# Performance work log

Hardware: AMD Instinct MI355X
Metric: run time of the kernel (lower is better)

## Reference

```python
import jax, jax.numpy as jnp
import numpy as np

EMBED_DIM = 1024
VALUE_DIM = 2048
NUM_HEADS = 8
KEY_DIM = EMBED_DIM // NUM_HEADS      # 128
HEAD_DIM = VALUE_DIM // NUM_HEADS     # 256
B, T = 2, 2048
EPS = 1e-6


def _rotate_every_two(x):
    # x: [..., d] with d even; pairs (x0,x1)->(-x1,x0)
    x1 = x[..., ::2]
    x2 = x[..., 1::2]
    return jnp.stack((-x2, x1), axis=-1).reshape(x.shape)


def _theta_shift(x, sin, cos):
    # sin/cos: [T, key_dim] broadcast over [B, H, T, key_dim]
    return x * cos + _rotate_every_two(x) * sin


def setup_inputs() -> dict:
    key = jax.random.key(0)
    ks = jax.random.split(key, 6)
    x = jax.random.normal(ks[0], (B, T, EMBED_DIM), dtype=jnp.float32)

    # rotary angles as in torchscale RetNetRelPos
    angle = 1.0 / (10000.0 ** jnp.linspace(0.0, 1.0, KEY_DIM // 2))
    angle = jnp.repeat(angle, 2)                       # [key_dim], interleaved pairs
    idx = jnp.arange(T, dtype=jnp.float32)
    sin = jnp.sin(idx[:, None] * angle[None, :])       # [T, key_dim]
    cos = jnp.cos(idx[:, None] * angle[None, :])

    # per-head decay mask, normalized by sqrt(row-sum) as in RetNet
    decay = jnp.log(1.0 - 2.0 ** (-5.0 - jnp.arange(NUM_HEADS, dtype=jnp.float32)))
    diff = idx[:, None] - idx[None, :]                 # [T, T]
    exponent = jnp.where(diff >= 0, decay[:, None, None] * diff[None], -jnp.inf)
    mask = jnp.exp(exponent)                           # [H, T, T], lower-triangular decay
    mask = mask / jnp.sqrt(mask.sum(-1, keepdims=True))

    s = 0.02
    Wq = s * jax.random.normal(ks[1], (EMBED_DIM, EMBED_DIM), dtype=jnp.float32)
    Wk = s * jax.random.normal(ks[2], (EMBED_DIM, EMBED_DIM), dtype=jnp.float32)
    Wv = s * jax.random.normal(ks[3], (EMBED_DIM, VALUE_DIM), dtype=jnp.float32)
    Wg = s * jax.random.normal(ks[4], (EMBED_DIM, VALUE_DIM), dtype=jnp.float32)
    Wo = s * jax.random.normal(ks[5], (VALUE_DIM, EMBED_DIM), dtype=jnp.float32)
    return {"x": x, "sin": sin, "cos": cos, "mask": mask,
            "Wq": Wq, "Wk": Wk, "Wv": Wv, "Wg": Wg, "Wo": Wo}


def reference(x, sin, cos, mask, Wq, Wk, Wv, Wg, Wo):
    bsz, tgt_len, _ = x.shape
    scaling = KEY_DIM ** (-0.5)

    q = x @ Wq
    k = (x @ Wk) * scaling
    v = x @ Wv
    g = x @ Wg

    q = q.reshape(bsz, tgt_len, NUM_HEADS, KEY_DIM).transpose(0, 2, 1, 3)  # [B,H,T,kd]
    k = k.reshape(bsz, tgt_len, NUM_HEADS, KEY_DIM).transpose(0, 2, 1, 3)
    qr = _theta_shift(q, sin, cos)
    kr = _theta_shift(k, sin, cos)

    vr = v.reshape(bsz, tgt_len, NUM_HEADS, HEAD_DIM).transpose(0, 2, 1, 3)  # [B,H,T,hd]

    # parallel retention: decay-masked QK^T with abs-sum normalization (detached)
    qk = jnp.einsum('bhtd,bhsd->bhts', qr, kr) * mask[None]
    denom = jnp.clip(jnp.sum(jnp.abs(jax.lax.stop_gradient(qk)), axis=-1, keepdims=True),
                     1.0, 50000.0)
    qk = qk / denom
    out = jnp.einsum('bhts,bhsd->bhtd', qk, vr)          # [B,H,T,hd]
    out = out.transpose(0, 2, 1, 3)                      # [B,T,H,hd]

    # per-head RMSNorm (no affine)
    out = out * jax.lax.rsqrt(jnp.mean(out * out, axis=-1, keepdims=True) + EPS)
    out = out.reshape(bsz, tgt_len, VALUE_DIM)

    out = jax.nn.silu(g) * out
    return out @ Wo
```

## Files before the change

### kernel.cpp

```cpp
#include <hip/hip_runtime.h>
#include <hip/hip_bf16.h>
#include <math.h>

constexpr int T_SEQ = 2048;
constexpr int BB    = 2;
constexpr int EMBED = 1024;
constexpr int VDIM  = 2048;
constexpr int NHEADS = 8;
constexpr int KDIM  = 128;
constexpr int HDIM  = 256;
constexpr int ROWS  = BB * T_SEQ;
constexpr int NALL  = 6144;
constexpr float EPS = 1e-6f;

typedef float  f32x4  __attribute__((ext_vector_type(4)));
typedef __bf16 bf16x8 __attribute__((ext_vector_type(8)));
typedef __bf16 bf16x4 __attribute__((ext_vector_type(4)));

__device__ __forceinline__ void gload16(const void* g, void* l) {
    __builtin_amdgcn_global_load_lds(
        (__attribute__((address_space(1))) void*)g,
        (__attribute__((address_space(3))) void*)l, 16, 0, 0);
}

__global__ __launch_bounds__(256)
void f32_to_bf16(const float* __restrict__ in, __bf16* __restrict__ out, int n4) {
    int i = blockIdx.x * 256 + threadIdx.x;
    if (i < n4) {
        float4 v = reinterpret_cast<const float4*>(in)[i];
        bf16x4 o = { (__bf16)v.x, (__bf16)v.y, (__bf16)v.z, (__bf16)v.w };
        reinterpret_cast<bf16x4*>(out)[i] = o;
    }
}

__global__ __launch_bounds__(256)
void transpose_all(const float* __restrict__ Wq, const float* __restrict__ Wk,
                   const float* __restrict__ Wv, const float* __restrict__ Wg,
                   const float* __restrict__ Wo,
                   __bf16* __restrict__ WqT, __bf16* __restrict__ WkT,
                   __bf16* __restrict__ WvT, __bf16* __restrict__ WgT,
                   __bf16* __restrict__ WoT) {
    const int bid = blockIdx.x;
    const float* W; __bf16* WT; int K, N, cx, cy;
    if (bid < 1024)      { W = Wq; WT = WqT; K = 1024; N = 1024; int rm = bid;        cx = rm & 31; cy = rm >> 5; }
    else if (bid < 2048) { W = Wk; WT = WkT; K = 1024; N = 1024; int rm = bid - 1024; cx = rm & 31; cy = rm >> 5; }
    else if (bid < 4096) { W = Wv; WT = WvT; K = 1024; N = 2048; int rm = bid - 2048; cx = rm & 63; cy = rm >> 6; }
    else if (bid < 6144) { W = Wg; WT = WgT; K = 1024; N = 2048; int rm = bid - 4096; cx = rm & 63; cy = rm >> 6; }
    else                 { W = Wo; WT = WoT; K = 2048; N = 1024; int rm = bid - 6144; cx = rm & 31; cy = rm >> 5; }

    __shared__ float tile[32][33];
    const int c0 = cx * 32, k0 = cy * 32;
    const int x = threadIdx.x, y = threadIdx.y;
    #pragma unroll
    for (int p = 0; p < 4; ++p)
        tile[y + p * 8][x] = W[(size_t)(k0 + y + p * 8) * N + c0 + x];
    __syncthreads();
    #pragma unroll
    for (int p = 0; p < 4; ++p)
        WT[(size_t)(c0 + y + p * 8) * K + k0 + x] = (__bf16)tile[x][y + p * 8];
}

__global__ __launch_bounds__(256)
void gemm_qkvg(const __bf16* __restrict__ A, const __bf16* __restrict__ BT,
               __bf16* __restrict__ Qb, __bf16* __restrict__ Kb,
               __bf16* __restrict__ Vt, __bf16* __restrict__ Gb,
               const float* __restrict__ sinT, const float* __restrict__ cosT) {
    constexpr int K = EMBED;
    __shared__ __align__(16) char smem[4 * 64 * 72 * 2];
    __bf16* As = (__bf16*)smem;
    __bf16* Bs = (__bf16*)(smem + 8192);

    const int bid = blockIdx.x;
    const int swzb = (bid & 7) * 192 + (bid >> 3);
    const int rowBase = (swzb / 48) * 128;
    const int colBase = (swzb % 48) * 128;

    const int tid = threadIdx.x;
    const int w = tid >> 6, lane = tid & 63;
    const int g = lane >> 4, r = lane & 15;
    const int wm = w >> 1, wn = w & 1;

    const int swz = ((lane & 3) ^ ((lane >> 3) & 3)) * 8;
    const int lr  = lane >> 2;
    const __bf16* aS0 = A  + (size_t)(rowBase + 32 * w      + lr) * K + swz;
    const __bf16* aS1 = A  + (size_t)(rowBase + 32 * w + 16 + lr) * K + swz;
    const __bf16* bS0 = BT + (size_t)(colBase + 32 * w      + lr) * K + swz;
    const __bf16* bS1 = BT + (size_t)(colBase + 32 * w + 16 + lr) * K + swz;
    char* aD0 = smem        + (2 * w    ) * 1024;
    char* aD1 = smem        + (2 * w + 1) * 1024;
    char* bD0 = smem + 8192 + (2 * w    ) * 1024;
    char* bD1 = smem + 8192 + (2 * w + 1) * 1024;

    const int colR = (g ^ ((r >> 1) & 3)) * 8;

    f32x4 acc[4][4];
    #pragma unroll
    for (int i = 0; i < 4; ++i)
        #pragma unroll
        for (int j = 0; j < 4; ++j)
            acc[i][j] = (f32x4){0.f, 0.f, 0.f, 0.f};

    for (int k0 = 0; k0 < K; k0 += 32) {
        __syncthreads();
        gload16(aS0 + k0, aD0);
        gload16(aS1 + k0, aD1);
        gload16(bS0 + k0, bD0);
        gload16(bS1 + k0, bD1);
        __syncthreads();

        bf16x8 bfrag[4];
        #pragma unroll
        for (int nf = 0; nf < 4; ++nf)
            bfrag[nf] = *reinterpret_cast<const bf16x8*>(
                &Bs[(wn * 64 + nf * 16 + r) * 32 + colR]);
        #pragma unroll
        for (int mf = 0; mf < 4; ++mf) {
            bf16x8 a = *reinterpret_cast<const bf16x8*>(
                &As[(wm * 64 + mf * 16 + r) * 32 + colR]);
            #pragma unroll
            for (int nf = 0; nf < 4; ++nf)
                acc[mf][nf] = __builtin_amdgcn_mfma_f32_16x16x32_bf16(a, bfrag[nf], acc[mf][nf], 0, 0, 0);
        }
    }

    constexpr float kscale = 0.08838834764831845f;
    if (colBase >= 2048 && colBase < 4096) {
        __syncthreads();
        __bf16* Es = (__bf16*)smem + w * (64 * 72);
        #pragma unroll
        for (int mf = 0; mf < 4; ++mf)
            #pragma unroll
            for (int nf = 0; nf < 4; ++nf) {
                bf16x4 v = { (__bf16)acc[mf][nf][0], (__bf16)acc[mf][nf][1],
                             (__bf16)acc[mf][nf][2], (__bf16)acc[mf][nf][3] };
                *reinterpret_cast<bf16x4*>(&Es[(nf * 16 + r) * 72 + mf * 16 + g * 4]) = v;
            }
        __syncthreads();
        const int t0g = rowBase + wm * 64;
        const int bq = t0g >> 11, tl = t0g & 2047;
        const int colV0 = (colBase - 2048) + wn * 64;
        const int h = colV0 >> 8, d0 = colV0 & 255;
        const int li = lane & 7, rgrp = lane >> 3;
        __bf16* vtb = Vt + ((size_t)(bq * NHEADS + h) * HDIM + d0) * T_SEQ + tl;
        #pragma unroll
        for (int c = 0; c < 8; ++c) {
            const int drow = 8 * c + rgrp;
            bf16x8 v = *reinterpret_cast<const bf16x8*>(&Es[drow * 72 + li * 8]);
            *reinterpret_cast<bf16x8*>(vtb + (size_t)drow * T_SEQ + li * 8) = v;
        }
        return;
    }

    __bf16* dst; int dstride, cofs; float alphaSeg; bool rot;
    if (colBase < 1024)      { dst = Qb; dstride = 1024; cofs = colBase;        alphaSeg = 1.0f;   rot = true;  }
    else if (colBase < 2048) { dst = Kb; dstride = 1024; cofs = colBase - 1024; alphaSeg = kscale; rot = true;  }
    else                     { dst = Gb; dstride = 2048; cofs = colBase - 4096; alphaSeg = 1.0f;   rot = false; }

    #pragma unroll
    for (int mf = 0; mf < 4; ++mf)
        #pragma unroll
        for (int nf = 0; nf < 4; ++nf)
            #pragma unroll
            for (int j = 0; j < 4; ++j) {
                const int row  = rowBase + wm * 64 + mf * 16 + g * 4 + j;
                const int colL = cofs + wn * 64 + nf * 16 + r;
                float v = acc[mf][nf][j] * alphaSeg;
                if (rot) {
                    const float p = __shfl_xor(v, 1);
                    const int t  = row & (T_SEQ - 1);
                    const int dh = colL & (KDIM - 1);
                    const float c = cosT[t * KDIM + dh];
                    const float s = sinT[t * KDIM + dh];
                    v = (r & 1) ? (v * c + p * s) : (v * c - p * s);
                }
                dst[(size_t)row * dstride + colL] = (__bf16)v;
            }
}

__global__ __launch_bounds__(256)
void gemm_wo(const __bf16* __restrict__ A, const __bf16* __restrict__ BT,
             float* __restrict__ C) {
    constexpr int N = EMBED, K = VDIM;
    __shared__ __align__(16) __bf16 As[64 * 32];
    __shared__ __align__(16) __bf16 Bs[128 * 32];

    const int bid = blockIdx.x;
    const int swzb = (bid & 7) * 64 + (bid >> 3);
    const int rowBase = (swzb >> 3) * 64;
    const int colBase = (swzb & 7) * 128;

    const int tid = threadIdx.x;
    const int w = tid >> 6, lane = tid & 63;
    const int g = lane >> 4, r = lane & 15;
    const int wm = w >> 1, wn = w & 1;

    const int swz = ((lane & 3) ^ ((lane >> 3) & 3)) * 8;
    const int lr  = lane >> 2;
    const __bf16* aS  = A  + (size_t)(rowBase + 16 * w + lr) * K + swz;
    const __bf16* bS0 = BT + (size_t)(colBase + 32 * w      + lr) * K + swz;
    const __bf16* bS1 = BT + (size_t)(colBase + 32 * w + 16 + lr) * K + swz;
    char* aD  = (char*)&As[0] + w * 1024;
    char* bD0 = (char*)&Bs[0] + (2 * w    ) * 1024;
    char* bD1 = (char*)&Bs[0] + (2 * w + 1) * 1024;

    const int colR = (g ^ ((r >> 1) & 3)) * 8;

    f32x4 acc[2][4];
    #pragma unroll
    for (int i = 0; i < 2; ++i)
        #pragma unroll
        for (int j = 0; j < 4; ++j)
            acc[i][j] = (f32x4){0.f, 0.f, 0.f, 0.f};

    for (int k0 = 0; k0 < K; k0 += 32) {
        __syncthreads();
        gload16(aS  + k0, aD);
        gload16(bS0 + k0, bD0);
        gload16(bS1 + k0, bD1);
        __syncthreads();

        bf16x8 bfrag[4];
        #pragma unroll
        for (int nf = 0; nf < 4; ++nf)
            bfrag[nf] = *reinterpret_cast<const bf16x8*>(
                &Bs[(wn * 64 + nf * 16 + r) * 32 + colR]);
        #pragma unroll
        for (int mf = 0; mf < 2; ++mf) {
            bf16x8 a = *reinterpret_cast<const bf16x8*>(
                &As[(wm * 32 + mf * 16 + r) * 32 + colR]);
            #pragma unroll
            for (int nf = 0; nf < 4; ++nf)
                acc[mf][nf] = __builtin_amdgcn_mfma_f32_16x16x32_bf16(a, bfrag[nf], acc[mf][nf], 0, 0, 0);
        }
    }

    #pragma unroll
    for (int mf = 0; mf < 2; ++mf)
        #pragma unroll
        for (int nf = 0; nf < 4; ++nf)
            #pragma unroll
            for (int j = 0; j < 4; ++j) {
                const int row = rowBase + wm * 32 + mf * 16 + g * 4 + j;
                const int col = colBase + wn * 64 + nf * 16 + r;
                C[(size_t)row * N + col] = acc[mf][nf][j];
            }
}

__global__ __launch_bounds__(256)
void retention_mfma(const __bf16* __restrict__ Qb, const __bf16* __restrict__ Kb,
                    const __bf16* __restrict__ Vt,
                    const __bf16* __restrict__ Gb, __bf16* __restrict__ Yb) {
    const int tid = threadIdx.x;
    const int w = tid >> 6, lane = tid & 63;
    const int g = lane >> 4, r = lane & 15;
    const int rx = r & 7;
    const int bid = blockIdx.x;
    const int h = bid & 7;
    const int slot = bid >> 3;
    const int b = slot & 1;
    const int x = slot >> 1;
    const int qt = (b == 0) ? (31 - x) : x;
    const int tt0 = qt * 64;
    const int trow0 = w * 16;

    __shared__ __align__(16) __bf16 Ks[64][128];
    __shared__ __align__(16) __bf16 Vs[256][64];
    __shared__ __align__(16) __bf16 Ps[4][16][72];

    const float rho   = 1.0f - exp2f(-(float)(5 + h));
    const float l2r   = log2f(rho);
    const float inv1m = exp2f((float)(5 + h));
    int   tj[4];
    float nrm[4];
    #pragma unroll
    for (int j = 0; j < 4; ++j) {
        tj[j] = tt0 + trow0 + g * 4 + j;
        nrm[j] = rsqrtf((1.0f - exp2f(l2r * (float)(tj[j] + 1))) * inv1m);
    }
    float pneg[4];
    #pragma unroll
    for (int ssub = 0; ssub < 4; ++ssub)
        pneg[ssub] = exp2f(-l2r * (float)(ssub * 16 + r));

    bf16x8 qf[4];
    {
        const __bf16* qrow = Qb + ((size_t)(b * T_SEQ + tt0 + trow0 + r)) * EMBED + h * KDIM;
        #pragma unroll
        for (int kb = 0; kb < 4; ++kb)
            qf[kb] = *reinterpret_cast<const bf16x8*>(qrow + kb * 32 + g * 8);
    }

    f32x4 acc[16];
    #pragma unroll
    for (int db = 0; db < 16; ++db) acc[db] = (f32x4){0.f, 0.f, 0.f, 0.f};
    float dsum[4] = {0.f, 0.f, 0.f, 0.f};

    const __bf16* vtbase = Vt + ((size_t)(b * NHEADS + h) * HDIM) * T_SEQ;
    const __bf16* kbase  = Kb + ((size_t)(b * T_SEQ)) * EMBED + h * KDIM;

    const int klr = lane >> 4;
    const int kc  = lane & 15;
    const int kswz_even = (kc ^ klr) * 8;
    const int kswz_odd  = (kc ^ (4 + klr)) * 8;
    const int vlr  = lane >> 3;
    const int vswz = ((lane & 7) ^ vlr) * 8;

    const int nS = qt + 1;
    for (int st = 0; st < nS; ++st) {
        const int ss0 = st * 64;
        __syncthreads();
        #pragma unroll
        for (int p = 0; p < 4; ++p) {
            const int cc = 4 * w + p;
            const int se = (p & 1) ? kswz_odd : kswz_even;
            gload16(kbase + (size_t)(ss0 + 4 * cc + klr) * EMBED + se,
                    (char*)&Ks[0][0] + cc * 1024);
        }
        #pragma unroll
        for (int p = 0; p < 8; ++p) {
            const int cc = 8 * w + p;
            gload16(vtbase + (size_t)(8 * cc + vlr) * T_SEQ + ss0 + vswz,
                    (char*)&Vs[0][0] + cc * 1024);
        }
        __syncthreads();

        float wj[4];
        #pragma unroll
        for (int j = 0; j < 4; ++j)
            wj[j] = exp2f(l2r * (float)(tj[j] - ss0)) * nrm[j];
        const bool diag = (st == qt);

        #pragma unroll
        for (int ssub = 0; ssub < 4; ++ssub) {
            f32x4 sacc = (f32x4){0.f, 0.f, 0.f, 0.f};
            #pragma unroll
            for (int kb = 0; kb < 4; ++kb) {
                bf16x8 kf = *reinterpret_cast<const bf16x8*>(
                    &Ks[ssub * 16 + r][((kb * 4 + g) ^ rx) * 8]);
                sacc = __builtin_amdgcn_mfma_f32_16x16x32_bf16(qf[kb], kf, sacc, 0, 0, 0);
            }
            const int scol = ss0 + ssub * 16 + r;
            const float mfac = pneg[ssub];
            #pragma unroll
            for (int j = 0; j < 4; ++j) {
                float pv = sacc[j] * (wj[j] * mfac);
                if (diag && scol > tj[j]) pv = 0.f;
                dsum[j] += fabsf(pv);
                Ps[w][g * 4 + j][ssub * 16 + r] = (__bf16)pv;
            }
        }

        #pragma unroll
        for (int sh = 0; sh < 2; ++sh) {
            bf16x8 pf = *reinterpret_cast<const bf16x8*>(&Ps[w][r][sh * 32 + g * 8]);
            #pragma unroll
            for (int db = 0; db < 16; ++db) {
                bf16x8 vf = *reinterpret_cast<const bf16x8*>(
                    &Vs[db * 16 + r][((sh * 4 + g) ^ rx) * 8]);
                acc[db] = __builtin_amdgcn_mfma_f32_16x16x32_bf16(pf, vf, acc[db], 0, 0, 0);
            }
        }
    }

    #pragma unroll
    for (int j = 0; j < 4; ++j) {
        float v = dsum[j];
        v += __shfl_xor(v, 1); v += __shfl_xor(v, 2);
        v += __shfl_xor(v, 4); v += __shfl_xor(v, 8);
        dsum[j] = fminf(fmaxf(v, 1.0f), 50000.0f);
    }
    float ss[4] = {0.f, 0.f, 0.f, 0.f};
    #pragma unroll
    for (int db = 0; db < 16; ++db)
        #pragma unroll
        for (int j = 0; j < 4; ++j) {
            const float v = acc[db][j] / dsum[j];
            acc[db][j] = v;
            ss[j] = fmaf(v, v, ss[j]);
        }
    #pragma unroll
    for (int j = 0; j < 4; ++j) {
        float v = ss[j];
        v += __shfl_xor(v, 1); v += __shfl_xor(v, 2);
        v += __shfl_xor(v, 4); v += __shfl_xor(v, 8);
        ss[j] = rsqrtf(v * (1.0f / 256.0f) + EPS);
    }
    #pragma unroll
    for (int j = 0; j < 4; ++j) {
        const size_t row = (size_t)(b * T_SEQ + tj[j]);
        const __bf16* grow = Gb + row * VDIM + h * HDIM;
        __bf16* yrow = Yb + row * VDIM + h * HDIM;
        #pragma unroll
        for (int db = 0; db < 16; ++db) {
            const int c = db * 16 + r;
            const float gv = (float)grow[c];
            const float sil = gv / (1.0f + expf(-gv));
            yrow[c] = (__bf16)(sil * acc[db][j] * ss[j]);
        }
    }
}

extern "C" void kernel_launch(void* const* d_in, const int* in_sizes, int n_in,
                              void* d_out, int out_size, void* d_ws, size_t ws_size,
                              hipStream_t stream) {
    (void)in_sizes; (void)n_in; (void)out_size; (void)ws_size;

    const float* x    = (const float*)d_in[0];
    const float* sinT = (const float*)d_in[1];
    const float* cosT = (const float*)d_in[2];
    const float* Wq   = (const float*)d_in[4];
    const float* Wk   = (const float*)d_in[5];
    const float* Wv   = (const float*)d_in[6];
    const float* Wg   = (const float*)d_in[7];
    const float* Wo   = (const float*)d_in[8];
    float* out = (float*)d_out;

    char* wsp = (char*)d_ws;
    __bf16* xb  = (__bf16*)(wsp);
    __bf16* WqT = (__bf16*)(wsp + (8u  << 20));
    __bf16* WkT = (__bf16*)(wsp + (10u << 20));
    __bf16* WvT = (__bf16*)(wsp + (12u << 20));
    __bf16* WgT = (__bf16*)(wsp + (16u << 20));
    __bf16* WoT = (__bf16*)(wsp + (20u << 20));
    __bf16* Qb  = (__bf16*)(wsp + (24u << 20));
    __bf16* Kb  = (__bf16*)(wsp + (32u << 20));
    __bf16* Yb  = (__bf16*)(wsp + (40u << 20));
    __bf16* Gb  = (__bf16*)(wsp + (56u << 20));
    __bf16* Vt  = (__bf16*)(wsp + (72u << 20));
    __bf16* WTall = WqT;

    const dim3 blk(256);
    const dim3 tblk(32, 8);

    f32_to_bf16<<<(ROWS * EMBED / 4) / 256, blk, 0, stream>>>(x, xb, ROWS * EMBED / 4);
    transpose_all<<<8192, tblk, 0, stream>>>(Wq, Wk, Wv, Wg, Wo, WqT, WkT, WvT, WgT, WoT);

    gemm_qkvg<<<1536, blk, 0, stream>>>(xb, WTall, Qb, Kb, Vt, Gb, sinT, cosT);

    retention_mfma<<<512, blk, 0, stream>>>(Qb, Kb, Vt, Gb, Yb);

    gemm_wo<<<512, blk, 0, stream>>>(Yb, WoT, out);
}
```

Before: 192.9 us.

## Add 4-stage async LDS pipeline to projection GEMMs with vmcnt waits

```diff
diff --git a/kernel.cpp b/kernel.cpp
--- a/kernel.cpp
+++ b/kernel.cpp
@@ -22,6 +22,9 @@
         (__attribute__((address_space(1))) void*)g,
         (__attribute__((address_space(3))) void*)l, 16, 0, 0);
 }
+
+#define WAITV(n) asm volatile("s_waitcnt vmcnt(" #n ")" ::: "memory")
+#define BARRIER() __builtin_amdgcn_s_barrier()
 
 __global__ __launch_bounds__(256)
 void f32_to_bf16(const float* __restrict__ in, __bf16* __restrict__ out, int n4) {
@@ -66,14 +69,11 @@
                __bf16* __restrict__ Vt, __bf16* __restrict__ Gb,
                const float* __restrict__ sinT, const float* __restrict__ cosT) {
     constexpr int K = EMBED;
-    __shared__ __align__(16) char smem[4 * 64 * 72 * 2];
-    __bf16* As = (__bf16*)smem;
-    __bf16* Bs = (__bf16*)(smem + 8192);
-
-    const int bid = blockIdx.x;
-    const int swzb = (bid & 7) * 192 + (bid >> 3);
-    const int rowBase = (swzb / 48) * 128;
-    const int colBase = (swzb % 48) * 128;
+    constexpr int NT = K / 32;
+    __shared__ __align__(16) char smem[4 * 16384];
+
+    const int rowBase = blockIdx.y * 128;
+    const int colBase = blockIdx.x * 128;
 
     const int tid = threadIdx.x;
     const int w = tid >> 6, lane = tid & 63;
@@ -86,10 +86,7 @@
     const __bf16* aS1 = A  + (size_t)(rowBase + 32 * w + 16 + lr) * K + swz;
     const __bf16* bS0 = BT + (size_t)(colBase + 32 * w      + lr) * K + swz;
     const __bf16* bS1 = BT + (size_t)(colBase + 32 * w + 16 + lr) * K + swz;
-    char* aD0 = smem        + (2 * w    ) * 1024;
-    char* aD1 = smem        + (2 * w + 1) * 1024;
-    char* bD0 = smem + 8192 + (2 * w    ) * 1024;
-    char* bD1 = smem + 8192 + (2 * w + 1) * 1024;
+    const int d0 = (2 * w) * 1024, d1 = (2 * w + 1) * 1024;
 
     const int colR = (g ^ ((r >> 1) & 3)) * 8;
 
@@ -100,28 +97,44 @@
         for (int j = 0; j < 4; ++j)
             acc[i][j] = (f32x4){0.f, 0.f, 0.f, 0.f};
 
-    for (int k0 = 0; k0 < K; k0 += 32) {
-        __syncthreads();
-        gload16(aS0 + k0, aD0);
-        gload16(aS1 + k0, aD1);
-        gload16(bS0 + k0, bD0);
-        gload16(bS1 + k0, bD1);
-        __syncthreads();
-
+    auto STAGE = [&](int t) {
+        char* bb = smem + (t & 3) * 16384;
+        const int ks = t * 32;
+        gload16(aS0 + ks, bb + d0);
+        gload16(aS1 + ks, bb + d1);
+        gload16(bS0 + ks, bb + 8192 + d0);
+        gload16(bS1 + ks, bb + 8192 + d1);
+    };
+    auto COMPUTE = [&](int t) {
+        const __bf16* Asb = (const __bf16*)(smem + (t & 3) * 16384);
+        const __bf16* Bsb = Asb + 4096;
         bf16x8 bfrag[4];
         #pragma unroll
         for (int nf = 0; nf < 4; ++nf)
             bfrag[nf] = *reinterpret_cast<const bf16x8*>(
-                &Bs[(wn * 64 + nf * 16 + r) * 32 + colR]);
+                &Bsb[(wn * 64 + nf * 16 + r) * 32 + colR]);
+        __builtin_amdgcn_s_setprio(1);
         #pragma unroll
         for (int mf = 0; mf < 4; ++mf) {
             bf16x8 a = *reinterpret_cast<const bf16x8*>(
-                &As[(wm * 64 + mf * 16 + r) * 32 + colR]);
+                &Asb[(wm * 64 + mf * 16 + r) * 32 + colR]);
             #pragma unroll
             for (int nf = 0; nf < 4; ++nf)
                 acc[mf][nf] = __builtin_amdgcn_mfma_f32_16x16x32_bf16(a, bfrag[nf], acc[mf][nf], 0, 0, 0);
         }
-    }
+        __builtin_amdgcn_s_setprio(0);
+    };
+
+    STAGE(0); STAGE(1); STAGE(2);
+    for (int t = 0; t < NT - 3; ++t) {
+        WAITV(8);
+        BARRIER();
+        STAGE(t + 3);
+        COMPUTE(t);
+    }
+    WAITV(8); BARRIER(); COMPUTE(NT - 3);
+    WAITV(4); BARRIER(); COMPUTE(NT - 2);
+    WAITV(0); BARRIER(); COMPUTE(NT - 1);
 
     constexpr float kscale = 0.08838834764831845f;
     if (colBase >= 2048 && colBase < 4096) {
@@ -139,9 +152,9 @@
         const int t0g = rowBase + wm * 64;
         const int bq = t0g >> 11, tl = t0g & 2047;
         const int colV0 = (colBase - 2048) + wn * 64;
-        const int h = colV0 >> 8, d0 = colV0 & 255;
+        const int h = colV0 >> 8, dd0 = colV0 & 255;
         const int li = lane & 7, rgrp = lane >> 3;
-        __bf16* vtb = Vt + ((size_t)(bq * NHEADS + h) * HDIM + d0) * T_SEQ + tl;
+        __bf16* vtb = Vt + ((size_t)(bq * NHEADS + h) * HDIM + dd0) * T_SEQ + tl;
         #pragma unroll
         for (int c = 0; c < 8; ++c) {
             const int drow = 8 * c + rgrp;
@@ -181,8 +194,8 @@
 void gemm_wo(const __bf16* __restrict__ A, const __bf16* __restrict__ BT,
              float* __restrict__ C) {
     constexpr int N = EMBED, K = VDIM;
-    __shared__ __align__(16) __bf16 As[64 * 32];
-    __shared__ __align__(16) __bf16 Bs[128 * 32];
+    constexpr int NT = K / 32;
+    __shared__ __align__(16) char smem[4 * 12288];
 
     const int bid = blockIdx.x;
     const int swzb = (bid & 7) * 64 + (bid >> 3);
@@ -199,9 +212,8 @@
     const __bf16* aS  = A  + (size_t)(rowBase + 16 * w + lr) * K + swz;
     const __bf16* bS0 = BT + (size_t)(colBase + 32 * w      + lr) * K + swz;
     const __bf16* bS1 = BT + (size_t)(colBase + 32 * w + 16 + lr) * K + swz;
-    char* aD  = (char*)&As[0] + w * 1024;
-    char* bD0 = (char*)&Bs[0] + (2 * w    ) * 1024;
-    char* bD1 = (char*)&Bs[0] + (2 * w + 1) * 1024;
+    const int ad = w * 1024;
+    const int d0 = (2 * w) * 1024, d1 = (2 * w + 1) * 1024;
 
     const int colR = (g ^ ((r >> 1) & 3)) * 8;
 
@@ -212,27 +224,43 @@
         for (int j = 0; j < 4; ++j)
             acc[i][j] = (f32x4){0.f, 0.f, 0.f, 0.f};
 
-    for (int k0 = 0; k0 < K; k0 += 32) {
-        __syncthreads();
-        gload16(aS  + k0, aD);
-        gload16(bS0 + k0, bD0);
-        gload16(bS1 + k0, bD1);
-        __syncthreads();
-
+    auto STAGE = [&](int t) {
+        char* bb = smem + (t & 3) * 12288;
+        const int ks = t * 32;
+        gload16(aS  + ks, bb + ad);
+        gload16(bS0 + ks, bb + 4096 + d0);
+        gload16(bS1 + ks, bb + 4096 + d1);
+    };
+    auto COMPUTE = [&](int t) {
+        const __bf16* Asb = (const __bf16*)(smem + (t & 3) * 12288);
+        const __bf16* Bsb = Asb + 2048;
         bf16x8 bfrag[4];
         #pragma unroll
         for (int nf = 0; nf < 4; ++nf)
             bfrag[nf] = *reinterpret_cast<const bf16x8*>(
-                &Bs[(wn * 64 + nf * 16 + r) * 32 + colR]);
+                &Bsb[(wn * 64 + nf * 16 + r) * 32 + colR]);
+        __builtin_amdgcn_s_setprio(1);
         #pragma unroll
         for (int mf = 0; mf < 2; ++mf) {
             bf16x8 a = *reinterpret_cast<const bf16x8*>(
-                &As[(wm * 32 + mf * 16 + r) * 32 + colR]);
+                &Asb[(wm * 32 + mf * 16 + r) * 32 + colR]);
             #pragma unroll
             for (int nf = 0; nf < 4; ++nf)
                 acc[mf][nf] = __builtin_amdgcn_mfma_f32_16x16x32_bf16(a, bfrag[nf], acc[mf][nf], 0, 0, 0);
         }
-    }
+        __builtin_amdgcn_s_setprio(0);
+    };
+
+    STAGE(0); STAGE(1); STAGE(2);
+    for (int t = 0; t < NT - 3; ++t) {
+        WAITV(6);
+        BARRIER();
+        STAGE(t + 3);
+        COMPUTE(t);
+    }
+    WAITV(6); BARRIER(); COMPUTE(NT - 3);
+    WAITV(3); BARRIER(); COMPUTE(NT - 2);
+    WAITV(0); BARRIER(); COMPUTE(NT - 1);
 
     #pragma unroll
     for (int mf = 0; mf < 2; ++mf)
@@ -435,7 +463,8 @@
     f32_to_bf16<<<(ROWS * EMBED / 4) / 256, blk, 0, stream>>>(x, xb, ROWS * EMBED / 4);
     transpose_all<<<8192, tblk, 0, stream>>>(Wq, Wk, Wv, Wg, Wo, WqT, WkT, WvT, WgT, WoT);
 
-    gemm_qkvg<<<1536, blk, 0, stream>>>(xb, WTall, Qb, Kb, Vt, Gb, sinT, cosT);
+    gemm_qkvg<<<dim3(NALL / 128, ROWS / 128), blk, 0, stream>>>(
+        xb, WTall, Qb, Kb, Vt, Gb, sinT, cosT);
 
     retention_mfma<<<512, blk, 0, stream>>>(Qb, Kb, Vt, Gb, Yb);
 
```

Result: slower. 204.1 us (+5.8%).

## Split PV product across waves by head-dim instead of query rows

Applied to the files above, without the earlier changes.

```diff
diff --git a/kernel.cpp b/kernel.cpp
--- a/kernel.cpp
+++ b/kernel.cpp
@@ -139,9 +139,9 @@
         const int t0g = rowBase + wm * 64;
         const int bq = t0g >> 11, tl = t0g & 2047;
         const int colV0 = (colBase - 2048) + wn * 64;
-        const int h = colV0 >> 8, d0 = colV0 & 255;
+        const int h = colV0 >> 8, dd0 = colV0 & 255;
         const int li = lane & 7, rgrp = lane >> 3;
-        __bf16* vtb = Vt + ((size_t)(bq * NHEADS + h) * HDIM + d0) * T_SEQ + tl;
+        __bf16* vtb = Vt + ((size_t)(bq * NHEADS + h) * HDIM + dd0) * T_SEQ + tl;
         #pragma unroll
         for (int c = 0; c < 8; ++c) {
             const int drow = 8 * c + rgrp;
@@ -265,7 +265,9 @@
 
     __shared__ __align__(16) __bf16 Ks[64][128];
     __shared__ __align__(16) __bf16 Vs[256][64];
-    __shared__ __align__(16) __bf16 Ps[4][16][72];
+    __shared__ __align__(16) __bf16 Ps[64][72];
+    __shared__ float dsumL[64];
+    __shared__ float ssL[4][64];
 
     const float rho   = 1.0f - exp2f(-(float)(5 + h));
     const float l2r   = log2f(rho);
@@ -290,9 +292,12 @@
             qf[kb] = *reinterpret_cast<const bf16x8*>(qrow + kb * 32 + g * 8);
     }
 
-    f32x4 acc[16];
-    #pragma unroll
-    for (int db = 0; db < 16; ++db) acc[db] = (f32x4){0.f, 0.f, 0.f, 0.f};
+    f32x4 acc[4][4];
+    #pragma unroll
+    for (int qs = 0; qs < 4; ++qs)
+        #pragma unroll
+        for (int ds = 0; ds < 4; ++ds)
+            acc[qs][ds] = (f32x4){0.f, 0.f, 0.f, 0.f};
     float dsum[4] = {0.f, 0.f, 0.f, 0.f};
 
     const __bf16* vtbase = Vt + ((size_t)(b * NHEADS + h) * HDIM) * T_SEQ;
@@ -346,18 +351,25 @@
                 float pv = sacc[j] * (wj[j] * mfac);
                 if (diag && scol > tj[j]) pv = 0.f;
                 dsum[j] += fabsf(pv);
-                Ps[w][g * 4 + j][ssub * 16 + r] = (__bf16)pv;
-            }
-        }
+                Ps[trow0 + g * 4 + j][ssub * 16 + r] = (__bf16)pv;
+            }
+        }
+        __syncthreads();
 
         #pragma unroll
         for (int sh = 0; sh < 2; ++sh) {
-            bf16x8 pf = *reinterpret_cast<const bf16x8*>(&Ps[w][r][sh * 32 + g * 8]);
-            #pragma unroll
-            for (int db = 0; db < 16; ++db) {
+            bf16x8 pf[4];
+            #pragma unroll
+            for (int qs = 0; qs < 4; ++qs)
+                pf[qs] = *reinterpret_cast<const bf16x8*>(
+                    &Ps[qs * 16 + r][sh * 32 + g * 8]);
+            #pragma unroll
+            for (int ds = 0; ds < 4; ++ds) {
                 bf16x8 vf = *reinterpret_cast<const bf16x8*>(
-                    &Vs[db * 16 + r][((sh * 4 + g) ^ rx) * 8]);
-                acc[db] = __builtin_amdgcn_mfma_f32_16x16x32_bf16(pf, vf, acc[db], 0, 0, 0);
+                    &Vs[w * 64 + ds * 16 + r][((sh * 4 + g) ^ rx) * 8]);
+                #pragma unroll
+                for (int qs = 0; qs < 4; ++qs)
+                    acc[qs][ds] = __builtin_amdgcn_mfma_f32_16x16x32_bf16(pf[qs], vf, acc[qs][ds], 0, 0, 0);
             }
         }
     }
@@ -369,35 +381,49 @@
         v += __shfl_xor(v, 4); v += __shfl_xor(v, 8);
         dsum[j] = fminf(fmaxf(v, 1.0f), 50000.0f);
     }
-    float ss[4] = {0.f, 0.f, 0.f, 0.f};
-    #pragma unroll
-    for (int db = 0; db < 16; ++db)
+    if (r == 0) {
+        #pragma unroll
+        for (int j = 0; j < 4; ++j)
+            dsumL[trow0 + g * 4 + j] = dsum[j];
+    }
+    __syncthreads();
+
+    #pragma unroll
+    for (int qs = 0; qs < 4; ++qs)
         #pragma unroll
         for (int j = 0; j < 4; ++j) {
-            const float v = acc[db][j] / dsum[j];
-            acc[db][j] = v;
-            ss[j] = fmaf(v, v, ss[j]);
-        }
-    #pragma unroll
-    for (int j = 0; j < 4; ++j) {
-        float v = ss[j];
-        v += __shfl_xor(v, 1); v += __shfl_xor(v, 2);
-        v += __shfl_xor(v, 4); v += __shfl_xor(v, 8);
-        ss[j] = rsqrtf(v * (1.0f / 256.0f) + EPS);
-    }
-    #pragma unroll
-    for (int j = 0; j < 4; ++j) {
-        const size_t row = (size_t)(b * T_SEQ + tj[j]);
-        const __bf16* grow = Gb + row * VDIM + h * HDIM;
-        __bf16* yrow = Yb + row * VDIM + h * HDIM;
-        #pragma unroll
-        for (int db = 0; db < 16; ++db) {
-            const int c = db * 16 + r;
-            const float gv = (float)grow[c];
-            const float sil = gv / (1.0f + expf(-gv));
-            yrow[c] = (__bf16)(sil * acc[db][j] * ss[j]);
-        }
-    }
+            const float inv = 1.0f / dsumL[qs * 16 + g * 4 + j];
+            float sp = 0.f;
+            #pragma unroll
+            for (int ds = 0; ds < 4; ++ds) {
+                const float v = acc[qs][ds][j] * inv;
+                acc[qs][ds][j] = v;
+                sp = fmaf(v, v, sp);
+            }
+            sp += __shfl_xor(sp, 1); sp += __shfl_xor(sp, 2);
+            sp += __shfl_xor(sp, 4); sp += __shfl_xor(sp, 8);
+            if (r == 0) ssL[w][qs * 16 + g * 4 + j] = sp;
+        }
+    __syncthreads();
+
+    #pragma unroll
+    for (int qs = 0; qs < 4; ++qs)
+        #pragma unroll
+        for (int j = 0; j < 4; ++j) {
+            const int ql = qs * 16 + g * 4 + j;
+            const float tot = ssL[0][ql] + ssL[1][ql] + ssL[2][ql] + ssL[3][ql];
+            const float rs = rsqrtf(tot * (1.0f / 256.0f) + EPS);
+            const size_t row = (size_t)(b * T_SEQ + tt0 + ql);
+            const __bf16* grow = Gb + row * VDIM + h * HDIM;
+            __bf16* yrow = Yb + row * VDIM + h * HDIM;
+            #pragma unroll
+            for (int ds = 0; ds < 4; ++ds) {
+                const int c = w * 64 + ds * 16 + r;
+                const float gv = (float)grow[c];
+                const float sil = gv / (1.0f + expf(-gv));
+                yrow[c] = (__bf16)(sil * acc[qs][ds][j] * rs);
+            }
+        }
 }
 
 extern "C" void kernel_launch(void* const* d_in, const int* in_sizes, int n_in,
```

Result: slower. 244.8 us (+26.9%).

## Double GEMM K-tile to 64 with XOR-swizzled LDS and merge prep kernels

Applied to the files above, without the earlier changes.

```diff
diff --git a/kernel.cpp b/kernel.cpp
--- a/kernel.cpp
+++ b/kernel.cpp
@@ -24,23 +24,22 @@
 }
 
 __global__ __launch_bounds__(256)
-void f32_to_bf16(const float* __restrict__ in, __bf16* __restrict__ out, int n4) {
-    int i = blockIdx.x * 256 + threadIdx.x;
-    if (i < n4) {
-        float4 v = reinterpret_cast<const float4*>(in)[i];
+void prep_all(const float* __restrict__ x, const float* __restrict__ Wq,
+              const float* __restrict__ Wk, const float* __restrict__ Wv,
+              const float* __restrict__ Wg, const float* __restrict__ Wo,
+              __bf16* __restrict__ xb,
+              __bf16* __restrict__ WqT, __bf16* __restrict__ WkT,
+              __bf16* __restrict__ WvT, __bf16* __restrict__ WgT,
+              __bf16* __restrict__ WoT) {
+    const int bid = blockIdx.x;
+    const int x_ = threadIdx.x, y_ = threadIdx.y;
+    if (bid >= 8192) {
+        const int i = (bid - 8192) * 256 + y_ * 32 + x_;
+        float4 v = reinterpret_cast<const float4*>(x)[i];
         bf16x4 o = { (__bf16)v.x, (__bf16)v.y, (__bf16)v.z, (__bf16)v.w };
-        reinterpret_cast<bf16x4*>(out)[i] = o;
-    }
-}
-
-__global__ __launch_bounds__(256)
-void transpose_all(const float* __restrict__ Wq, const float* __restrict__ Wk,
-                   const float* __restrict__ Wv, const float* __restrict__ Wg,
-                   const float* __restrict__ Wo,
-                   __bf16* __restrict__ WqT, __bf16* __restrict__ WkT,
-                   __bf16* __restrict__ WvT, __bf16* __restrict__ WgT,
-                   __bf16* __restrict__ WoT) {
-    const int bid = blockIdx.x;
+        reinterpret_cast<bf16x4*>(xb)[i] = o;
+        return;
+    }
     const float* W; __bf16* WT; int K, N, cx, cy;
     if (bid < 1024)      { W = Wq; WT = WqT; K = 1024; N = 1024; int rm = bid;        cx = rm & 31; cy = rm >> 5; }
     else if (bid < 2048) { W = Wk; WT = WkT; K = 1024; N = 1024; int rm = bid - 1024; cx = rm & 31; cy = rm >> 5; }
@@ -50,14 +49,13 @@
 
     __shared__ float tile[32][33];
     const int c0 = cx * 32, k0 = cy * 32;
-    const int x = threadIdx.x, y = threadIdx.y;
     #pragma unroll
     for (int p = 0; p < 4; ++p)
-        tile[y + p * 8][x] = W[(size_t)(k0 + y + p * 8) * N + c0 + x];
+        tile[y_ + p * 8][x_] = W[(size_t)(k0 + y_ + p * 8) * N + c0 + x_];
     __syncthreads();
     #pragma unroll
     for (int p = 0; p < 4; ++p)
-        WT[(size_t)(c0 + y + p * 8) * K + k0 + x] = (__bf16)tile[x][y + p * 8];
+        WT[(size_t)(c0 + y_ + p * 8) * K + k0 + x_] = (__bf16)tile[x_][y_ + p * 8];
 }
 
 __global__ __launch_bounds__(256)
@@ -66,9 +64,9 @@
                __bf16* __restrict__ Vt, __bf16* __restrict__ Gb,
                const float* __restrict__ sinT, const float* __restrict__ cosT) {
     constexpr int K = EMBED;
-    __shared__ __align__(16) char smem[4 * 64 * 72 * 2];
+    __shared__ __align__(16) char smem[36864];
     __bf16* As = (__bf16*)smem;
-    __bf16* Bs = (__bf16*)(smem + 8192);
+    __bf16* Bs = (__bf16*)(smem + 16384);
 
     const int bid = blockIdx.x;
     const int swzb = (bid & 7) * 192 + (bid >> 3);
@@ -80,18 +78,10 @@
     const int g = lane >> 4, r = lane & 15;
     const int wm = w >> 1, wn = w & 1;
 
-    const int swz = ((lane & 3) ^ ((lane >> 3) & 3)) * 8;
-    const int lr  = lane >> 2;
-    const __bf16* aS0 = A  + (size_t)(rowBase + 32 * w      + lr) * K + swz;
-    const __bf16* aS1 = A  + (size_t)(rowBase + 32 * w + 16 + lr) * K + swz;
-    const __bf16* bS0 = BT + (size_t)(colBase + 32 * w      + lr) * K + swz;
-    const __bf16* bS1 = BT + (size_t)(colBase + 32 * w + 16 + lr) * K + swz;
-    char* aD0 = smem        + (2 * w    ) * 1024;
-    char* aD1 = smem        + (2 * w + 1) * 1024;
-    char* bD0 = smem + 8192 + (2 * w    ) * 1024;
-    char* bD1 = smem + 8192 + (2 * w + 1) * 1024;
-
-    const int colR = (g ^ ((r >> 1) & 3)) * 8;
+    const int vr  = lane >> 3;
+    const int swz = ((lane & 7) ^ vr) * 8;
+    const __bf16* aSb = A  + (size_t)(rowBase + 32 * w + vr) * K + swz;
+    const __bf16* bSb = BT + (size_t)(colBase + 32 * w + vr) * K + swz;
 
     f32x4 acc[4][4];
     #pragma unroll
@@ -100,26 +90,34 @@
         for (int j = 0; j < 4; ++j)
             acc[i][j] = (f32x4){0.f, 0.f, 0.f, 0.f};
 
-    for (int k0 = 0; k0 < K; k0 += 32) {
-        __syncthreads();
-        gload16(aS0 + k0, aD0);
-        gload16(aS1 + k0, aD1);
-        gload16(bS0 + k0, bD0);
-        gload16(bS1 + k0, bD1);
-        __syncthreads();
-
-        bf16x8 bfrag[4];
-        #pragma unroll
-        for (int nf = 0; nf < 4; ++nf)
-            bfrag[nf] = *reinterpret_cast<const bf16x8*>(
-                &Bs[(wn * 64 + nf * 16 + r) * 32 + colR]);
-        #pragma unroll
-        for (int mf = 0; mf < 4; ++mf) {
-            bf16x8 a = *reinterpret_cast<const bf16x8*>(
-                &As[(wm * 64 + mf * 16 + r) * 32 + colR]);
-            #pragma unroll
-            for (int nf = 0; nf < 4; ++nf)
-                acc[mf][nf] = __builtin_amdgcn_mfma_f32_16x16x32_bf16(a, bfrag[nf], acc[mf][nf], 0, 0, 0);
+    for (int k0 = 0; k0 < K; k0 += 64) {
+        __syncthreads();
+        #pragma unroll
+        for (int p = 0; p < 4; ++p) {
+            const int cc = 4 * w + p;
+            gload16(aSb + (size_t)(8 * p) * K + k0, smem         + cc * 1024);
+            gload16(bSb + (size_t)(8 * p) * K + k0, smem + 16384 + cc * 1024);
+        }
+        __syncthreads();
+
+        #pragma unroll
+        for (int kk = 0; kk < 2; ++kk) {
+            bf16x8 bfrag[4];
+            #pragma unroll
+            for (int nf = 0; nf < 4; ++nf) {
+                const int row = wn * 64 + nf * 16 + r;
+                bfrag[nf] = *reinterpret_cast<const bf16x8*>(
+                    &Bs[row * 64 + (((kk << 2) + g) ^ (r & 7)) * 8]);
+            }
+            #pragma unroll
+            for (int mf = 0; mf < 4; ++mf) {
+                const int row = wm * 64 + mf * 16 + r;
+                bf16x8 a = *reinterpret_cast<const bf16x8*>(
+                    &As[row * 64 + (((kk << 2) + g) ^ (r & 7)) * 8]);
+                #pragma unroll
+                for (int nf = 0; nf < 4; ++nf)
+                    acc[mf][nf] = __builtin_amdgcn_mfma_f32_16x16x32_bf16(a, bfrag[nf], acc[mf][nf], 0, 0, 0);
+            }
         }
     }
 
@@ -139,9 +137,9 @@
         const int t0g = rowBase + wm * 64;
         const int bq = t0g >> 11, tl = t0g & 2047;
         const int colV0 = (colBase - 2048) + wn * 64;
-        const int h = colV0 >> 8, d0 = colV0 & 255;
+        const int h = colV0 >> 8, dd0 = colV0 & 255;
         const int li = lane & 7, rgrp = lane >> 3;
-        __bf16* vtb = Vt + ((size_t)(bq * NHEADS + h) * HDIM + d0) * T_SEQ + tl;
+        __bf16* vtb = Vt + ((size_t)(bq * NHEADS + h) * HDIM + dd0) * T_SEQ + tl;
         #pragma unroll
         for (int c = 0; c < 8; ++c) {
             const int drow = 8 * c + rgrp;
@@ -181,8 +179,9 @@
 void gemm_wo(const __bf16* __restrict__ A, const __bf16* __restrict__ BT,
              float* __restrict__ C) {
     constexpr int N = EMBED, K = VDIM;
-    __shared__ __align__(16) __bf16 As[64 * 32];
-    __shared__ __align__(16) __bf16 Bs[128 * 32];
+    __shared__ __align__(16) char smem[24576];
+    __bf16* As = (__bf16*)smem;
+    __bf16* Bs = (__bf16*)(smem + 8192);
 
     const int bid = blockIdx.x;
     const int swzb = (bid & 7) * 64 + (bid >> 3);
@@ -194,16 +193,10 @@
     const int g = lane >> 4, r = lane & 15;
     const int wm = w >> 1, wn = w & 1;
 
-    const int swz = ((lane & 3) ^ ((lane >> 3) & 3)) * 8;
-    const int lr  = lane >> 2;
-    const __bf16* aS  = A  + (size_t)(rowBase + 16 * w + lr) * K + swz;
-    const __bf16* bS0 = BT + (size_t)(colBase + 32 * w      + lr) * K + swz;
-    const __bf16* bS1 = BT + (size_t)(colBase + 32 * w + 16 + lr) * K + swz;
-    char* aD  = (char*)&As[0] + w * 1024;
-    char* bD0 = (char*)&Bs[0] + (2 * w    ) * 1024;
-    char* bD1 = (char*)&Bs[0] + (2 * w + 1) * 1024;
-
-    const int colR = (g ^ ((r >> 1) & 3)) * 8;
+    const int vr  = lane >> 3;
+    const int swz = ((lane & 7) ^ vr) * 8;
+    const __bf16* aSb = A  + (size_t)(rowBase + 16 * w + vr) * K + swz;
+    const __bf16* bSb = BT + (size_t)(colBase + 32 * w + vr) * K + swz;
 
     f32x4 acc[2][4];
     #pragma unroll
@@ -212,25 +205,38 @@
         for (int j = 0; j < 4; ++j)
             acc[i][j] = (f32x4){0.f, 0.f, 0.f, 0.f};
 
-    for (int k0 = 0; k0 < K; k0 += 32) {
-        __syncthreads();
-        gload16(aS  + k0, aD);
-        gload16(bS0 + k0, bD0);
-        gload16(bS1 + k0, bD1);
-        __syncthreads();
-
-        bf16x8 bfrag[4];
-        #pragma unroll
-        for (int nf = 0; nf < 4; ++nf)
-            bfrag[nf] = *reinterpret_cast<const bf16x8*>(
-                &Bs[(wn * 64 + nf * 16 + r) * 32 + colR]);
-        #pragma unroll
-        for (int mf = 0; mf < 2; ++mf) {
-            bf16x8 a = *reinterpret_cast<const bf16x8*>(
-                &As[(wm * 32 + mf * 16 + r) * 32 + colR]);
-            #pragma unroll
-            for (int nf = 0; nf < 4; ++nf)
-                acc[mf][nf] = __builtin_amdgcn_mfma_f32_16x16x32_bf16(a, bfrag[nf], acc[mf][nf], 0, 0, 0);
+    for (int k0 = 0; k0 < K; k0 += 64) {
+        __syncthreads();
+        #pragma unroll
+        for (int p = 0; p < 2; ++p) {
+            const int cc = 2 * w + p;
+            gload16(aSb + (size_t)(8 * p) * K + k0, smem + cc * 1024);
+        }
+        #pragma unroll
+        for (int p = 0; p < 4; ++p) {
+            const int cc = 4 * w + p;
+            gload16(bSb + (size_t)(8 * p) * K + k0, smem + 8192 + cc * 1024);
+        }
+        __syncthreads();
+
+        #pragma unroll
+        for (int kk = 0; kk < 2; ++kk) {
+            bf16x8 bfrag[4];
+            #pragma unroll
+            for (int nf = 0; nf < 4; ++nf) {
+                const int row = wn * 64 + nf * 16 + r;
+                bfrag[nf] = *reinterpret_cast<const bf16x8*>(
+                    &Bs[row * 64 + (((kk << 2) + g) ^ (r & 7)) * 8]);
+            }
+            #pragma unroll
+            for (int mf = 0; mf < 2; ++mf) {
+                const int row = wm * 32 + mf * 16 + r;
+                bf16x8 a = *reinterpret_cast<const bf16x8*>(
+                    &As[row * 64 + (((kk << 2) + g) ^ (r & 7)) * 8]);
+                #pragma unroll
+                for (int nf = 0; nf < 4; ++nf)
+                    acc[mf][nf] = __builtin_amdgcn_mfma_f32_16x16x32_bf16(a, bfrag[nf], acc[mf][nf], 0, 0, 0);
+            }
         }
     }
 
@@ -432,8 +438,8 @@
     const dim3 blk(256);
     const dim3 tblk(32, 8);
 
-    f32_to_bf16<<<(ROWS * EMBED / 4) / 256, blk, 0, stream>>>(x, xb, ROWS * EMBED / 4);
-    transpose_all<<<8192, tblk, 0, stream>>>(Wq, Wk, Wv, Wg, Wo, WqT, WkT, WvT, WgT, WoT);
+    prep_all<<<12288, tblk, 0, stream>>>(x, Wq, Wk, Wv, Wg, Wo,
+                                         xb, WqT, WkT, WvT, WgT, WoT);
 
     gemm_qkvg<<<1536, blk, 0, stream>>>(xb, WTall, Qb, Kb, Vt, Gb, sinT, cosT);
 
```

Result: no change. 194.7 us (+0.9%).
